# Kernel optimization log

Hardware: AMD Instinct MI355X
Metric: run time of the kernel (lower is better)

Reference implementation:

```python
import jax, jax.numpy as jnp
import numpy as np
import math

B, S, D, H, F, L = 16, 512, 1024, 16, 4096, 4
DK = D // H
NEG = -1e32


def _cosine_pe(max_len, d_model):
    # deterministic sin/cos table (the 0.1*randn init is fully overwritten for even d_model)
    pos = np.arange(max_len, dtype=np.float32)[:, None]
    div = np.exp(np.arange(0, d_model, 2, dtype=np.float32) * (-(math.log(10000.0) / d_model)))
    pe = np.zeros((max_len, d_model), dtype=np.float32)
    pe[:, 0::2] = np.sin(pos * div)
    pe[:, 1::2] = np.cos(pos * div)
    return jnp.asarray(pe)[None]  # [1, max_len, D]


def setup_inputs() -> dict:
    key = jax.random.key(0)
    ks = jax.random.split(key, 16)
    sc_d = 1.0 / math.sqrt(D)
    sc_f = 1.0 / math.sqrt(F)
    return {
        "q_embed_data": jax.random.normal(ks[0], (B, S, D), jnp.float32),
        "qa_embed_data": jax.random.normal(ks[1], (B, S, D), jnp.float32),
        "pe": _cosine_pe(S, D),
        "Wk": jax.random.normal(ks[2], (L, D, D), jnp.float32) * sc_d,
        "bk": jnp.zeros((L, D), jnp.float32),
        "Wv": jax.random.normal(ks[3], (L, D, D), jnp.float32) * sc_d,
        "bv": jnp.zeros((L, D), jnp.float32),
        "Wo": jax.random.normal(ks[4], (L, D, D), jnp.float32) * sc_d,
        "bo": jnp.zeros((L, D), jnp.float32),
        "ln1_g": jnp.ones((L, D), jnp.float32),
        "ln1_b": jnp.zeros((L, D), jnp.float32),
        "W1": jax.random.normal(ks[5], (L, D, F), jnp.float32) * sc_d,
        "b1": jnp.zeros((L, F), jnp.float32),
        "W2": jax.random.normal(ks[6], (L, F, D), jnp.float32) * sc_f,
        "b2": jnp.zeros((L, D), jnp.float32),
        "ln2_g": jnp.ones((L, D), jnp.float32),
        "ln2_b": jnp.zeros((L, D), jnp.float32),
    }


def _layer_norm(x, g, b, eps=1e-5):
    mu = jnp.mean(x, axis=-1, keepdims=True)
    var = jnp.var(x, axis=-1, keepdims=True)
    return (x - mu) * jax.lax.rsqrt(var + eps) * g + b


def _forward(q_embed_data, qa_embed_data, pe, Wk, bk, Wv, bv, Wo, bo,
             ln1_g, ln1_b, W1, b1, W2, b2, ln2_g, ln2_b):
    x = q_embed_data + pe[:, :S, :]
    y = qa_embed_data + pe[:, :S, :]  # values stay fixed across blocks
    # mask=0 in TransformerLayer: triu(k=0)==0 -> strictly-lower-triangular allowed
    allowed = jnp.tril(jnp.ones((S, S), bool), k=-1)  # [S, S]
    row_keep = (jnp.arange(S) > 0).astype(x.dtype)[None, None, :, None]  # zero_pad row 0
    scale = 1.0 / math.sqrt(DK)
    for l in range(L):
        # kq_same: q and k both use k_linear
        qk = (x @ Wk[l] + bk[l]).reshape(B, S, H, DK).transpose(0, 2, 1, 3)  # [B,H,S,DK]
        v = (y @ Wv[l] + bv[l]).reshape(B, S, H, DK).transpose(0, 2, 1, 3)
        scores = jnp.einsum('bhqd,bhkd->bhqk', qk, qk) * scale
        scores = jnp.where(allowed, scores, NEG)
        attn = jax.nn.softmax(scores, axis=-1) * row_keep  # zero_pad: first query row -> zeros
        ctx = jnp.einsum('bhqk,bhkd->bhqd', attn, v)
        ctx = ctx.transpose(0, 2, 1, 3).reshape(B, S, D)
        x = _layer_norm(x + (ctx @ Wo[l] + bo[l]), ln1_g[l], ln1_b[l])
        ffn = jax.nn.relu(x @ W1[l] + b1[l]) @ W2[l] + b2[l]
        x = _layer_norm(x + ffn, ln2_g[l], ln2_b[l])
    return x


def reference(q_embed_data, qa_embed_data, pe, Wk, bk, Wv, bv, Wo, bo,
              ln1_g, ln1_b, W1, b1, W2, b2, ln2_g, ln2_b):
    return _forward(q_embed_data, qa_embed_data, pe, Wk, bk, Wv, bv, Wo, bo,
                    ln1_g, ln1_b, W1, b1, W2, b2, ln2_g, ln2_b)
```

## Files before the change

### kernel.cpp

```cpp
#include <hip/hip_runtime.h>
#include <stdint.h>

typedef unsigned short u16;
typedef __bf16 bf16x8 __attribute__((ext_vector_type(8)));
typedef float f32x4 __attribute__((ext_vector_type(4)));

#define BDIM 16
#define SLEN 512
#define DMODEL 1024
#define NHEAD 16
#define DHEAD 64
#define FDIM 4096
#define NLAYER 4
#define ROWS (BDIM*SLEN)
#define KVT 64

__device__ __forceinline__ u16 f2b(float f) {
  uint32_t u = __builtin_bit_cast(uint32_t, f);
  u = (u + 0x7fffu + ((u >> 16) & 1u)) >> 16;
  return (u16)u;
}
__device__ __forceinline__ float b2f_lo(uint32_t u) {
  return __builtin_bit_cast(float, u << 16);
}
__device__ __forceinline__ float b2f_hi(uint32_t u) {
  return __builtin_bit_cast(float, u & 0xffff0000u);
}

__device__ __forceinline__ void gl_lds16(const void* g, void* l) {
  uint32_t loff = (uint32_t)(uintptr_t)l;
  __builtin_amdgcn_global_load_lds(
      (__attribute__((address_space(1))) uint32_t*)(uintptr_t)g,
      (__attribute__((address_space(3))) uint32_t*)loff,
      16, 0, 0);
}

__global__ __launch_bounds__(256) void prep_kernel(const float4* __restrict__ q,
                                                   const float4* __restrict__ qa,
                                                   const float4* __restrict__ pe,
                                                   float4* __restrict__ x,
                                                   u16* __restrict__ xb,
                                                   u16* __restrict__ yb) {
  int idx = blockIdx.x * 256 + threadIdx.x;
  int pidx = idx & (SLEN * DMODEL / 4 - 1);
  float4 qv = q[idx], av = qa[idx], pv = pe[pidx];
  float4 xv = make_float4(qv.x + pv.x, qv.y + pv.y, qv.z + pv.z, qv.w + pv.w);
  float4 yv = make_float4(av.x + pv.x, av.y + pv.y, av.z + pv.z, av.w + pv.w);
  x[idx] = xv;
  uint32_t x0 = (uint32_t)f2b(xv.x) | ((uint32_t)f2b(xv.y) << 16);
  uint32_t x1 = (uint32_t)f2b(xv.z) | ((uint32_t)f2b(xv.w) << 16);
  uint32_t y0 = (uint32_t)f2b(yv.x) | ((uint32_t)f2b(yv.y) << 16);
  uint32_t y1 = (uint32_t)f2b(yv.z) | ((uint32_t)f2b(yv.w) << 16);
  ((uint2*)xb)[idx] = make_uint2(x0, x1);
  ((uint2*)yb)[idx] = make_uint2(y0, y1);
}

__global__ __launch_bounds__(256) void transpose_f2b(const float* __restrict__ in,
                                                     u16* __restrict__ out,
                                                     int M, int N) {
  __shared__ float t[32][33];
  int tx = threadIdx.x & 31, ty = threadIdx.x >> 5;
  int m0 = blockIdx.y * 32, n0 = blockIdx.x * 32;
  #pragma unroll
  for (int i = 0; i < 32; i += 8) t[ty + i][tx] = in[(size_t)(m0 + ty + i) * N + n0 + tx];
  __syncthreads();
  #pragma unroll
  for (int i = 0; i < 32; i += 8) out[(size_t)(n0 + ty + i) * M + m0 + tx] = f2b(t[tx][ty + i]);
}

template<int BN, bool RELU, bool BF16OUT>
__global__ __launch_bounds__(512, 2) void gemm8p(const u16* __restrict__ Ap,
                                                 const u16* __restrict__ Bp,
                                                 const float* __restrict__ bias,
                                                 void* __restrict__ Cp,
                                                 int M, int N, int K) {
  constexpr int NBH = BN / 128;
  constexpr int NREP = BN / 64;
  constexpr int QN = NREP / 2;
  constexpr int HU = 8192;
  __shared__ __attribute__((aligned(16))) u16 lds[2][(2 + NBH) * HU];

  const int tid = threadIdx.x, wave = tid >> 6, lane = tid & 63;
  const int lg = lane >> 4, lc = lane & 15;
  const int wm = wave >> 2, wn = wave & 3;

  const int gx = gridDim.x;
  int nwg = gx * gridDim.y;
  int orig = blockIdx.y * gx + blockIdx.x;
  int qq = nwg >> 3, rr_ = nwg & 7;
  int xcd = orig & 7, ix = orig >> 3;
  int wg = (xcd < rr_ ? xcd * (qq + 1) : rr_ * (qq + 1) + (xcd - rr_) * qq) + ix;
  const int m0 = (wg / gx) * 256, n0 = (wg % gx) * BN;

  const int ldbyte = K * 2;
  const char* Ag = (const char*)Ap + (size_t)m0 * ldbyte;
  const char* Bg = (const char*)Bp + (size_t)n0 * ldbyte;

  int o1 = tid * 16, o2 = 8192 + tid * 16;
  int sr1 = o1 >> 7, sg1 = (((o1 >> 4) & 7) - sr1) & 7;
  int sr2 = o2 >> 7, sg2 = (((o2 >> 4) & 7) - sr2) & 7;
  const int soff1 = sr1 * ldbyte + sg1 * 16;
  const int soff2 = sr2 * ldbyte + sg2 * 16;
  const int NT = K >> 6;

  auto stageA = [&](int kt, int h, int buf) {
    const char* g = Ag + (size_t)h * 128 * ldbyte + (size_t)kt * 128;
    char* d = (char*)&lds[buf][h * HU] + wave * 1024;
    gl_lds16(g + soff1, d);
    gl_lds16(g + soff2, d + 8192);
  };
  auto stageB = [&](int kt, int h, int buf) {
    const char* g = Bg + (size_t)h * 128 * ldbyte + (size_t)kt * 128;
    char* d = (char*)&lds[buf][(2 + h) * HU] + wave * 1024;
    gl_lds16(g + soff1, d);
    gl_lds16(g + soff2, d + 8192);
  };

  const int bstart = wn * (BN / 4);
  const int bh = bstart >> 7, bc0 = bstart & 127;

  auto rdA = [&](const u16* base, int f, int kk) -> bf16x8 {
    int row = f * 16 + lc;
    return *(const bf16x8*)&base[row * 64 + (((kk * 4 + lg + row) & 7) << 3)];
  };
  auto rdB = [&](const u16* base, int jj, int kk) -> bf16x8 {
    int row = bc0 + jj * 16 + lc;
    return *(const bf16x8*)&base[row * 64 + (((kk * 4 + lg + row) & 7) << 3)];
  };

  f32x4 acc[8][NREP];
  #pragma unroll
  for (int f = 0; f < 8; f++)
    #pragma unroll
    for (int j = 0; j < NREP; j++) acc[f][j] = (f32x4){0.f, 0.f, 0.f, 0.f};

  stageA(0, 0, 0); stageA(0, 1, 0);
  stageB(0, 0, 0); if (NBH == 2) stageB(0, 1, 0);
  stageA(1, 0, 1); stageA(1, 1, 1);
  asm volatile("s_waitcnt vmcnt(4)\n\ts_barrier" ::: "memory");

  auto ktile = [&](int k, int buf) {
    const u16* Ab_ = &lds[buf][wm * HU];
    const u16* Bb_ = &lds[buf][(2 + bh) * HU];
    const int kn = (k + 1 < NT) ? k + 1 : NT - 1;
    const int k2 = (k + 2 < NT) ? k + 2 : NT - 1;
    bf16x8 a0[4][2], a1[4][2], b0[QN][2], b1[QN][2];

    #pragma unroll
    for (int f = 0; f < 4; f++) { a0[f][0] = rdA(Ab_, f, 0); a0[f][1] = rdA(Ab_, f, 1); }
    #pragma unroll
    for (int j = 0; j < QN; j++) { b0[j][0] = rdB(Bb_, j, 0); b0[j][1] = rdB(Bb_, j, 1); }
    stageB(kn, 0, buf ^ 1);
    asm volatile("s_barrier" ::: "memory");
    __builtin_amdgcn_s_setprio(1);
    #pragma unroll
    for (int f = 0; f < 4; f++)
      #pragma unroll
      for (int j = 0; j < QN; j++) {
        acc[f][j] = __builtin_amdgcn_mfma_f32_16x16x32_bf16(a0[f][0], b0[j][0], acc[f][j], 0, 0, 0);
        acc[f][j] = __builtin_amdgcn_mfma_f32_16x16x32_bf16(a0[f][1], b0[j][1], acc[f][j], 0, 0, 0);
      }
    __builtin_amdgcn_s_setprio(0);
    asm volatile("s_barrier" ::: "memory");

    #pragma unroll
    for (int f = 0; f < 4; f++) { a1[f][0] = rdA(Ab_, 4 + f, 0); a1[f][1] = rdA(Ab_, 4 + f, 1); }
    if (NBH == 2) stageB(kn, 1, buf ^ 1);
    asm volatile("s_barrier" ::: "memory");
    __builtin_amdgcn_s_setprio(1);
    #pragma unroll
    for (int f = 0; f < 4; f++)
      #pragma unroll
      for (int j = 0; j < QN; j++) {
        acc[4 + f][j] = __builtin_amdgcn_mfma_f32_16x16x32_bf16(a1[f][0], b0[j][0], acc[4 + f][j], 0, 0, 0);
        acc[4 + f][j] = __builtin_amdgcn_mfma_f32_16x16x32_bf16(a1[f][1], b0[j][1], acc[4 + f][j], 0, 0, 0);
      }
    __builtin_amdgcn_s_setprio(0);
    asm volatile("s_barrier" ::: "memory");

    #pragma unroll
    for (int j = 0; j < QN; j++) { b1[j][0] = rdB(Bb_, QN + j, 0); b1[j][1] = rdB(Bb_, QN + j, 1); }
    stageA(k2, 0, buf);
    asm volatile("s_barrier" ::: "memory");
    __builtin_amdgcn_s_setprio(1);
    #pragma unroll
    for (int f = 0; f < 4; f++)
      #pragma unroll
      for (int j = 0; j < QN; j++) {
        acc[4 + f][QN + j] = __builtin_amdgcn_mfma_f32_16x16x32_bf16(a1[f][0], b1[j][0], acc[4 + f][QN + j], 0, 0, 0);
        acc[4 + f][QN + j] = __builtin_amdgcn_mfma_f32_16x16x32_bf16(a1[f][1], b1[j][1], acc[4 + f][QN + j], 0, 0, 0);
      }
    __builtin_amdgcn_s_setprio(0);
    asm volatile("s_barrier" ::: "memory");

    stageA(k2, 1, buf);
    asm volatile("s_barrier" ::: "memory");
    __builtin_amdgcn_s_setprio(1);
    #pragma unroll
    for (int f = 0; f < 4; f++)
      #pragma unroll
      for (int j = 0; j < QN; j++) {
        acc[f][QN + j] = __builtin_amdgcn_mfma_f32_16x16x32_bf16(a0[f][0], b1[j][0], acc[f][QN + j], 0, 0, 0);
        acc[f][QN + j] = __builtin_amdgcn_mfma_f32_16x16x32_bf16(a0[f][1], b1[j][1], acc[f][QN + j], 0, 0, 0);
      }
    __builtin_amdgcn_s_setprio(0);
    asm volatile("s_waitcnt vmcnt(4)\n\ts_barrier" ::: "memory");
  };

  for (int k = 0; k < NT; k += 2) {
    ktile(k, 0);
    ktile(k + 1, 1);
  }

  #pragma unroll
  for (int f = 0; f < 8; f++) {
    int row = m0 + wm * 128 + f * 16 + lg * 4;
    #pragma unroll
    for (int j = 0; j < NREP; j++) {
      int col = n0 + bstart + j * 16 + lc;
      float bv = bias[col];
      #pragma unroll
      for (int t2 = 0; t2 < 4; t2++) {
        float v = acc[f][j][t2] + bv;
        if (RELU) v = fmaxf(v, 0.f);
        if (BF16OUT) ((u16*)Cp)[(size_t)(row + t2) * N + col] = f2b(v);
        else         ((float*)Cp)[(size_t)(row + t2) * N + col] = v;
      }
    }
  }
}

__global__ __launch_bounds__(256, 2) void gemm4w(const u16* __restrict__ Ap,
                                                 const u16* __restrict__ Bp,
                                                 const float* __restrict__ bias,
                                                 u16* __restrict__ Cp,
                                                 int M, int N, int K) {
  __shared__ __attribute__((aligned(16))) u16 As[2][128 * 64];
  __shared__ __attribute__((aligned(16))) u16 Bs[2][128 * 64];
  const int tid = threadIdx.x, wave = tid >> 6, lane = tid & 63;
  const int lg = lane >> 4, lc = lane & 15;
  const int wm = wave >> 1, wn = wave & 1;

  const int gx = gridDim.x;
  int nwg = gx * gridDim.y;
  int orig = blockIdx.y * gx + blockIdx.x;
  int qq = nwg >> 3, rr_ = nwg & 7;
  int xcd = orig & 7, ix = orig >> 3;
  int wg = (xcd < rr_ ? xcd * (qq + 1) : rr_ * (qq + 1) + (xcd - rr_) * qq) + ix;
  const int m0 = (wg / gx) * 128, n0 = (wg % gx) * 128;

  const int ldbyte = K * 2;
  const char* Ag = (const char*)Ap + (size_t)m0 * ldbyte;
  const char* Bg = (const char*)Bp + (size_t)n0 * ldbyte;
  const int NT = K >> 6;

  auto stage = [&](const char* gb, int kt, u16* lb) {
    #pragma unroll
    for (int c = 0; c < 4; c++) {
      int o = c * 4096 + tid * 16;
      int row = o >> 7;
      int g = (((o >> 4) & 7) - row) & 7;
      gl_lds16(gb + (size_t)row * ldbyte + (size_t)kt * 128 + g * 16,
               (char*)lb + c * 4096 + wave * 1024);
    }
  };
  auto rd = [&](const u16* base, int strip, int f, int kk) -> bf16x8 {
    int row = strip * 64 + f * 16 + lc;
    return *(const bf16x8*)&base[row * 64 + (((kk * 4 + lg + row) & 7) << 3)];
  };

  f32x4 acc[4][4];
  #pragma unroll
  for (int f = 0; f < 4; f++)
    #pragma unroll
    for (int n = 0; n < 4; n++) acc[f][n] = (f32x4){0.f, 0.f, 0.f, 0.f};

  stage(Ag, 0, As[0]); stage(Bg, 0, Bs[0]);
  stage(Ag, 1, As[1]); stage(Bg, 1, Bs[1]);
  asm volatile("s_waitcnt vmcnt(8)\n\ts_barrier" ::: "memory");

  for (int k = 0; k < NT; k++) {
    const int buf = k & 1;
    const int k2 = (k + 2 < NT) ? k + 2 : NT - 1;
    bf16x8 a[4][2], b[4][2];
    #pragma unroll
    for (int f = 0; f < 4; f++) { a[f][0] = rd(As[buf], wm, f, 0); a[f][1] = rd(As[buf], wm, f, 1); }
    #pragma unroll
    for (int n = 0; n < 4; n++) { b[n][0] = rd(Bs[buf], wn, n, 0); b[n][1] = rd(Bs[buf], wn, n, 1); }
    asm volatile("s_barrier" ::: "memory");
    __builtin_amdgcn_s_setprio(1);
    #pragma unroll
    for (int f = 0; f < 4; f++)
      #pragma unroll
      for (int n = 0; n < 2; n++) {
        acc[f][n] = __builtin_amdgcn_mfma_f32_16x16x32_bf16(a[f][0], b[n][0], acc[f][n], 0, 0, 0);
        acc[f][n] = __builtin_amdgcn_mfma_f32_16x16x32_bf16(a[f][1], b[n][1], acc[f][n], 0, 0, 0);
      }
    __builtin_amdgcn_s_setprio(0);
    asm volatile("s_barrier" ::: "memory");
    stage(Ag, k2, As[buf]);
    stage(Bg, k2, Bs[buf]);
    __builtin_amdgcn_s_setprio(1);
    #pragma unroll
    for (int f = 0; f < 4; f++)
      #pragma unroll
      for (int n = 2; n < 4; n++) {
        acc[f][n] = __builtin_amdgcn_mfma_f32_16x16x32_bf16(a[f][0], b[n][0], acc[f][n], 0, 0, 0);
        acc[f][n] = __builtin_amdgcn_mfma_f32_16x16x32_bf16(a[f][1], b[n][1], acc[f][n], 0, 0, 0);
      }
    __builtin_amdgcn_s_setprio(0);
    asm volatile("s_waitcnt vmcnt(8)\n\ts_barrier" ::: "memory");
  }

  #pragma unroll
  for (int f = 0; f < 4; f++) {
    int row = m0 + wm * 64 + f * 16 + lg * 4;
    #pragma unroll
    for (int n = 0; n < 4; n++) {
      int col = n0 + wn * 64 + n * 16 + lc;
      float bv = bias[col];
      #pragma unroll
      for (int r = 0; r < 4; r++)
        Cp[(size_t)(row + r) * N + col] = f2b(acc[f][n][r] + bv);
    }
  }
}

__global__ __launch_bounds__(256, 4) void attn_kernel(const u16* __restrict__ QK,
                                                      const u16* __restrict__ V,
                                                      u16* __restrict__ CTX) {
  __shared__ __attribute__((aligned(16))) u16 Ks[2][KVT * 64];
  __shared__ __attribute__((aligned(16))) u16 VTs[64 * 72];
  __shared__ __attribute__((aligned(16))) u16 Ps[4][16 * 72];
  const int qt = blockIdx.x, bh = blockIdx.y;
  const int b = bh >> 4, h = bh & 15;
  const char* Qg = (const char*)(QK + (size_t)b * SLEN * DMODEL + h * DHEAD);
  const char* Vg = (const char*)(V + (size_t)b * SLEN * DMODEL + h * DHEAD);
  const int tid = threadIdx.x, wave = tid >> 6, lane = tid & 63;
  const int lg = lane >> 4, lc = lane & 15;
  const int ktmax = qt;

  auto stageK = [&](int kt, int buf) {
    #pragma unroll
    for (int i = 0; i < 2; i++) {
      int o = i * 4096 + tid * 16;
      int row = o >> 7, slot = (o >> 4) & 7;
      int g = (slot - row) & 7;
      gl_lds16(Qg + (size_t)(kt * KVT + row) * (DMODEL * 2) + g * 16,
               (char*)Ks[buf] + i * 4096 + wave * 1024);
    }
  };
  const int vhi = lane >> 5, vls = lane & 31;
  const int vc_ = wave + 4 * vhi;
  auto loadV = [&](int kt, uint4 (&va)[2]) {
    const char* src = Vg + (size_t)(kt * KVT + 2 * vls) * (DMODEL * 2) + vc_ * 16;
    va[0] = *(const uint4*)src;
    va[1] = *(const uint4*)(src + DMODEL * 2);
  };
  auto writeVT = [&](const uint4 (&va)[2]) {
    u16 e0[8], e1[8];
    *(uint4*)e0 = va[0];
    *(uint4*)e1 = va[1];
    #pragma unroll
    for (int j = 0; j < 8; j++) {
      uint32_t pk = (uint32_t)e0[j] | ((uint32_t)e1[j] << 16);
      *(uint32_t*)&VTs[(8 * vc_ + j) * 72 + 2 * vls] = pk;
    }
  };

  uint4 vaA[2], vaB[2];
  const int qrow = qt * 64 + wave * 16 + lc;
  bf16x8 aq0 = *(const bf16x8*)(Qg + (size_t)qrow * (DMODEL * 2) + lg * 16);
  bf16x8 aq1 = *(const bf16x8*)(Qg + (size_t)qrow * (DMODEL * 2) + 64 + lg * 16);
  stageK(0, 0);
  loadV(0, vaA);
  stageK(ktmax > 0 ? 1 : 0, 1);
  asm volatile("s_waitcnt vmcnt(2)\n\ts_barrier" ::: "memory");

  float l_run[4] = {0.f, 0.f, 0.f, 0.f};
  f32x4 acc_o[4];
  #pragma unroll
  for (int n = 0; n < 4; n++) acc_o[n] = (f32x4){0.f, 0.f, 0.f, 0.f};

  auto iter = [&](int kt, int cur, uint4 (&vc)[2], uint4 (&vn)[2]) {
    const int kn = (kt + 1 <= ktmax) ? kt + 1 : ktmax;
    const int k2 = (kt + 2 <= ktmax) ? kt + 2 : ktmax;

    asm volatile("s_waitcnt vmcnt(2)" ::: "memory");
    __builtin_amdgcn_s_barrier();
    writeVT(vc);
    loadV(kn, vn);

    f32x4 sc[4];
    #pragma unroll
    for (int n = 0; n < 4; n++) sc[n] = (f32x4){0.f, 0.f, 0.f, 0.f};
    #pragma unroll
    for (int n = 0; n < 4; n++) {
      int row = n * 16 + lc;
      bf16x8 bk0 = *(const bf16x8*)&Ks[cur][row * 64 + (((lg + row) & 7) << 3)];
      bf16x8 bk1 = *(const bf16x8*)&Ks[cur][row * 64 + (((4 + lg + row) & 7) << 3)];
      sc[n] = __builtin_amdgcn_mfma_f32_16x16x32_bf16(aq0, bk0, sc[n], 0, 0, 0);
      sc[n] = __builtin_amdgcn_mfma_f32_16x16x32_bf16(aq1, bk1, sc[n], 0, 0, 0);
    }

    const int qbase = qt * 64 + wave * 16 + lg * 4;
    #pragma unroll
    for (int n = 0; n < 4; n++) {
      int kg = kt * KVT + n * 16 + lc;
      #pragma unroll
      for (int r = 0; r < 4; r++) {
        float e = __expf(fmaf(sc[n][r], 0.125f, -24.f));
        float p = (kg < qbase + r) ? e : 0.f;
        l_run[r] += p;
        Ps[wave][(lg * 4 + r) * 72 + n * 16 + lc] = f2b(p);
      }
    }

    asm volatile("s_waitcnt lgkmcnt(0)" ::: "memory");
    __builtin_amdgcn_s_barrier();
    stageK(k2, cur);

    bf16x8 ap0 = *(const bf16x8*)&Ps[wave][lc * 72 + lg * 8];
    bf16x8 ap1 = *(const bf16x8*)&Ps[wave][lc * 72 + 32 + lg * 8];
    #pragma unroll
    for (int n2 = 0; n2 < 4; n2++) {
      bf16x8 bv0 = *(const bf16x8*)&VTs[(n2 * 16 + lc) * 72 + lg * 8];
      bf16x8 bv1 = *(const bf16x8*)&VTs[(n2 * 16 + lc) * 72 + 32 + lg * 8];
      acc_o[n2] = __builtin_amdgcn_mfma_f32_16x16x32_bf16(ap0, bv0, acc_o[n2], 0, 0, 0);
      acc_o[n2] = __builtin_amdgcn_mfma_f32_16x16x32_bf16(ap1, bv1, acc_o[n2], 0, 0, 0);
    }
  };

  for (int kt = 0; kt <= ktmax; kt += 2) {
    iter(kt, 0, vaA, vaB);
    if (kt + 1 <= ktmax) iter(kt + 1, 1, vaB, vaA);
  }

  #pragma unroll
  for (int d = 1; d < 16; d <<= 1)
    #pragma unroll
    for (int r = 0; r < 4; r++) l_run[r] += __shfl_xor(l_run[r], d, 64);

  asm volatile("s_waitcnt vmcnt(0)" ::: "memory");
  #pragma unroll
  for (int n2 = 0; n2 < 4; n2++)
    #pragma unroll
    for (int r = 0; r < 4; r++) {
      int sq = qt * 64 + wave * 16 + lg * 4 + r;
      float v = (sq == 0) ? 0.f : acc_o[n2][r] / l_run[r];
      CTX[((size_t)b * SLEN + sq) * DMODEL + h * DHEAD + n2 * 16 + lc] = f2b(v);
    }
}

__global__ __launch_bounds__(256) void ln_kernel(const u16* __restrict__ tmp,
                                                 float* __restrict__ x,
                                                 u16* __restrict__ xb,
                                                 const float* __restrict__ gw,
                                                 const float* __restrict__ bw) {
  __shared__ float red[4], red2[4];
  const int row = blockIdx.x, t = threadIdx.x;
  const size_t base = (size_t)row * DMODEL + t * 4;
  float4 xv = *(const float4*)&x[base];
  uint2 tv = *(const uint2*)&tmp[base];
  float v[4];
  v[0] = xv.x + b2f_lo(tv.x); v[1] = xv.y + b2f_hi(tv.x);
  v[2] = xv.z + b2f_lo(tv.y); v[3] = xv.w + b2f_hi(tv.y);
  float s = v[0] + v[1] + v[2] + v[3];
  #pragma unroll
  for (int d = 1; d < 64; d <<= 1) s += __shfl_xor(s, d, 64);
  if ((t & 63) == 0) red[t >> 6] = s;
  __syncthreads();
  float mean = (red[0] + red[1] + red[2] + red[3]) * (1.f / DMODEL);
  float q2 = 0.f;
  #pragma unroll
  for (int i = 0; i < 4; i++) { float d_ = v[i] - mean; q2 += d_ * d_; }
  #pragma unroll
  for (int d = 1; d < 64; d <<= 1) q2 += __shfl_xor(q2, d, 64);
  if ((t & 63) == 0) red2[t >> 6] = q2;
  __syncthreads();
  float var = (red2[0] + red2[1] + red2[2] + red2[3]) * (1.f / DMODEL);
  float rs = rsqrtf(var + 1e-5f);
  float4 gv = *(const float4*)&gw[t * 4];
  float4 bv4 = *(const float4*)&bw[t * 4];
  float o0 = (v[0] - mean) * rs * gv.x + bv4.x;
  float o1 = (v[1] - mean) * rs * gv.y + bv4.y;
  float o2 = (v[2] - mean) * rs * gv.z + bv4.z;
  float o3 = (v[3] - mean) * rs * gv.w + bv4.w;
  *(float4*)&x[base] = make_float4(o0, o1, o2, o3);
  uint2 pk;
  pk.x = (uint32_t)f2b(o0) | ((uint32_t)f2b(o1) << 16);
  pk.y = (uint32_t)f2b(o2) | ((uint32_t)f2b(o3) << 16);
  *(uint2*)&xb[base] = pk;
}

__global__ __launch_bounds__(256) void copy_f4(const float4* __restrict__ src, float4* __restrict__ dst) {
  int i = blockIdx.x * 256 + threadIdx.x;
  dst[i] = src[i];
}

extern "C" void kernel_launch(void* const* d_in, const int* in_sizes, int n_in,
                              void* d_out, int out_size, void* d_ws, size_t ws_size,
                              hipStream_t stream) {
  (void)in_sizes; (void)n_in; (void)out_size; (void)ws_size;
  const float* q    = (const float*)d_in[0];
  const float* qa   = (const float*)d_in[1];
  const float* pe   = (const float*)d_in[2];
  const float* Wk   = (const float*)d_in[3];
  const float* bk   = (const float*)d_in[4];
  const float* Wv   = (const float*)d_in[5];
  const float* bv   = (const float*)d_in[6];
  const float* Wo   = (const float*)d_in[7];
  const float* bo   = (const float*)d_in[8];
  const float* ln1g = (const float*)d_in[9];
  const float* ln1b = (const float*)d_in[10];
  const float* W1   = (const float*)d_in[11];
  const float* b1   = (const float*)d_in[12];
  const float* W2   = (const float*)d_in[13];
  const float* b2   = (const float*)d_in[14];
  const float* ln2g = (const float*)d_in[15];
  const float* ln2b = (const float*)d_in[16];

  char* w = (char*)d_ws;
  float* x_f32 = (float*)w; w += (size_t)ROWS * DMODEL * 4;
  u16* xb   = (u16*)w; w += (size_t)ROWS * DMODEL * 2;
  u16* yb   = (u16*)w; w += (size_t)ROWS * DMODEL * 2;
  u16* qkb  = (u16*)w; w += (size_t)ROWS * DMODEL * 2;
  u16* vb   = (u16*)w; w += (size_t)ROWS * DMODEL * 2;
  u16* ctxb = (u16*)w; w += (size_t)ROWS * DMODEL * 2;
  u16* ffnb = (u16*)w; w += (size_t)ROWS * FDIM * 2;
  u16* WkT  = (u16*)w; w += (size_t)DMODEL * DMODEL * 2;
  u16* WvT  = (u16*)w; w += (size_t)DMODEL * DMODEL * 2;
  u16* WoT  = (u16*)w; w += (size_t)DMODEL * DMODEL * 2;
  u16* W1T  = (u16*)w; w += (size_t)DMODEL * FDIM * 2;
  u16* W2T  = (u16*)w; w += (size_t)DMODEL * FDIM * 2;
  u16* tmpb = qkb;

  prep_kernel<<<ROWS * DMODEL / 4 / 256, 256, 0, stream>>>(
      (const float4*)q, (const float4*)qa, (const float4*)pe, (float4*)x_f32, xb, yb);

  for (int l = 0; l < NLAYER; l++) {
    transpose_f2b<<<dim3(32, 32), 256, 0, stream>>>(Wk + (size_t)l * DMODEL * DMODEL, WkT, DMODEL, DMODEL);
    transpose_f2b<<<dim3(32, 32), 256, 0, stream>>>(Wv + (size_t)l * DMODEL * DMODEL, WvT, DMODEL, DMODEL);
    transpose_f2b<<<dim3(32, 32), 256, 0, stream>>>(Wo + (size_t)l * DMODEL * DMODEL, WoT, DMODEL, DMODEL);
    transpose_f2b<<<dim3(128, 32), 256, 0, stream>>>(W1 + (size_t)l * DMODEL * FDIM, W1T, DMODEL, FDIM);
    transpose_f2b<<<dim3(32, 128), 256, 0, stream>>>(W2 + (size_t)l * FDIM * DMODEL, W2T, FDIM, DMODEL);

    gemm4w<<<dim3(DMODEL / 128, ROWS / 128), 256, 0, stream>>>(
        xb, WkT, bk + l * DMODEL, qkb, ROWS, DMODEL, DMODEL);
    gemm4w<<<dim3(DMODEL / 128, ROWS / 128), 256, 0, stream>>>(
        yb, WvT, bv + l * DMODEL, vb, ROWS, DMODEL, DMODEL);
    attn_kernel<<<dim3(SLEN / 64, BDIM * NHEAD), 256, 0, stream>>>(qkb, vb, ctxb);
    gemm4w<<<dim3(DMODEL / 128, ROWS / 128), 256, 0, stream>>>(
        ctxb, WoT, bo + l * DMODEL, tmpb, ROWS, DMODEL, DMODEL);
    ln_kernel<<<ROWS, 256, 0, stream>>>(tmpb, x_f32, xb, ln1g + l * DMODEL, ln1b + l * DMODEL);
    gemm8p<256, true, true><<<dim3(FDIM / 256, ROWS / 256), 512, 0, stream>>>(
        xb, W1T, b1 + l * FDIM, ffnb, ROWS, FDIM, DMODEL);
    gemm4w<<<dim3(DMODEL / 128, ROWS / 128), 256, 0, stream>>>(
        ffnb, W2T, b2 + l * DMODEL, tmpb, ROWS, DMODEL, FDIM);
    ln_kernel<<<ROWS, 256, 0, stream>>>(tmpb, x_f32, xb, ln2g + l * DMODEL, ln2b + l * DMODEL);
  }
  copy_f4<<<ROWS * DMODEL / 4 / 256, 256, 0, stream>>>((const float4*)x_f32, (float4*)d_out);
}
```

Measured before the change: 1.188 ms.

## Triple-buffer B tiles in 8-wave GEMM and use it for FFN down-projection

The 8-wave ping-pong GEMM now keeps three LDS slots for the weight (B) tile instead of two, so B is prefetched two k-tiles ahead rather than one. Wait counts are adjusted to match the larger number of loads in flight. The FFN second GEMM (K=4096) moves from the 4-wave 128x128 kernel to this 8-wave 256x128 variant. The extra B buffer raises LDS use, which can lower occupancy, and the larger tile halves the workgroup count for the W2 GEMM.

Result: slower. 1.242 ms (+4.5%).

```diff
diff --git a/kernel.cpp b/kernel.cpp
--- a/kernel.cpp
+++ b/kernel.cpp
@@ -68,17 +68,19 @@
   for (int i = 0; i < 32; i += 8) out[(size_t)(n0 + ty + i) * M + m0 + tx] = f2b(t[tx][ty + i]);
 }
 
-template<int BN, bool RELU, bool BF16OUT>
-__global__ __launch_bounds__(512, 2) void gemm8p(const u16* __restrict__ Ap,
-                                                 const u16* __restrict__ Bp,
-                                                 const float* __restrict__ bias,
-                                                 void* __restrict__ Cp,
-                                                 int M, int N, int K) {
+template<int BN, bool RELU>
+__global__ __launch_bounds__(512, 2) void gemm8pd(const u16* __restrict__ Ap,
+                                                  const u16* __restrict__ Bp,
+                                                  const float* __restrict__ bias,
+                                                  u16* __restrict__ Cp,
+                                                  int M, int N, int K) {
   constexpr int NBH = BN / 128;
   constexpr int NREP = BN / 64;
   constexpr int QN = NREP / 2;
   constexpr int HU = 8192;
-  __shared__ __attribute__((aligned(16))) u16 lds[2][(2 + NBH) * HU];
+  constexpr int VW = (2 + NBH) * 2;
+  __shared__ __attribute__((aligned(16))) u16 ldsA[2][2 * HU];
+  __shared__ __attribute__((aligned(16))) u16 ldsB[3][NBH * HU];
 
   const int tid = threadIdx.x, wave = tid >> 6, lane = tid & 63;
   const int lg = lane >> 4, lc = lane & 15;
@@ -105,13 +107,13 @@
 
   auto stageA = [&](int kt, int h, int buf) {
     const char* g = Ag + (size_t)h * 128 * ldbyte + (size_t)kt * 128;
-    char* d = (char*)&lds[buf][h * HU] + wave * 1024;
+    char* d = (char*)&ldsA[buf][h * HU] + wave * 1024;
     gl_lds16(g + soff1, d);
     gl_lds16(g + soff2, d + 8192);
   };
-  auto stageB = [&](int kt, int h, int buf) {
+  auto stageB = [&](int kt, int h, int slot) {
     const char* g = Bg + (size_t)h * 128 * ldbyte + (size_t)kt * 128;
-    char* d = (char*)&lds[buf][(2 + h) * HU] + wave * 1024;
+    char* d = (char*)&ldsB[slot][h * HU] + wave * 1024;
     gl_lds16(g + soff1, d);
     gl_lds16(g + soff2, d + 8192);
   };
@@ -137,12 +139,13 @@
   stageA(0, 0, 0); stageA(0, 1, 0);
   stageB(0, 0, 0); if (NBH == 2) stageB(0, 1, 0);
   stageA(1, 0, 1); stageA(1, 1, 1);
-  asm volatile("s_waitcnt vmcnt(4)\n\ts_barrier" ::: "memory");
-
-  auto ktile = [&](int k, int buf) {
-    const u16* Ab_ = &lds[buf][wm * HU];
-    const u16* Bb_ = &lds[buf][(2 + bh) * HU];
-    const int kn = (k + 1 < NT) ? k + 1 : NT - 1;
+  stageB(1, 0, 1); if (NBH == 2) stageB(1, 1, 1);
+  if (VW == 8) asm volatile("s_waitcnt vmcnt(8)\n\ts_barrier" ::: "memory");
+  else         asm volatile("s_waitcnt vmcnt(6)\n\ts_barrier" ::: "memory");
+
+  auto ktile = [&](int k, int abuf, int bc, int b2) {
+    const u16* Ab_ = &ldsA[abuf][wm * HU];
+    const u16* Bb_ = &ldsB[bc][bh * HU];
     const int k2 = (k + 2 < NT) ? k + 2 : NT - 1;
     bf16x8 a0[4][2], a1[4][2], b0[QN][2], b1[QN][2];
 
@@ -150,7 +153,7 @@
     for (int f = 0; f < 4; f++) { a0[f][0] = rdA(Ab_, f, 0); a0[f][1] = rdA(Ab_, f, 1); }
     #pragma unroll
     for (int j = 0; j < QN; j++) { b0[j][0] = rdB(Bb_, j, 0); b0[j][1] = rdB(Bb_, j, 1); }
-    stageB(kn, 0, buf ^ 1);
+    stageB(k2, 0, b2);
     asm volatile("s_barrier" ::: "memory");
     __builtin_amdgcn_s_setprio(1);
     #pragma unroll
@@ -165,7 +168,7 @@
 
     #pragma unroll
     for (int f = 0; f < 4; f++) { a1[f][0] = rdA(Ab_, 4 + f, 0); a1[f][1] = rdA(Ab_, 4 + f, 1); }
-    if (NBH == 2) stageB(kn, 1, buf ^ 1);
+    if (NBH == 2) stageB(k2, 1, b2);
     asm volatile("s_barrier" ::: "memory");
     __builtin_amdgcn_s_setprio(1);
     #pragma unroll
@@ -180,7 +183,7 @@
 
     #pragma unroll
     for (int j = 0; j < QN; j++) { b1[j][0] = rdB(Bb_, QN + j, 0); b1[j][1] = rdB(Bb_, QN + j, 1); }
-    stageA(k2, 0, buf);
+    stageA(k2, 0, abuf);
     asm volatile("s_barrier" ::: "memory");
     __builtin_amdgcn_s_setprio(1);
     #pragma unroll
@@ -193,7 +196,7 @@
     __builtin_amdgcn_s_setprio(0);
     asm volatile("s_barrier" ::: "memory");
 
-    stageA(k2, 1, buf);
+    stageA(k2, 1, abuf);
     asm volatile("s_barrier" ::: "memory");
     __builtin_amdgcn_s_setprio(1);
     #pragma unroll
@@ -204,12 +207,15 @@
         acc[f][QN + j] = __builtin_amdgcn_mfma_f32_16x16x32_bf16(a0[f][1], b1[j][1], acc[f][QN + j], 0, 0, 0);
       }
     __builtin_amdgcn_s_setprio(0);
-    asm volatile("s_waitcnt vmcnt(4)\n\ts_barrier" ::: "memory");
-  };
-
-  for (int k = 0; k < NT; k += 2) {
-    ktile(k, 0);
-    ktile(k + 1, 1);
+    if (VW == 8) asm volatile("s_waitcnt vmcnt(8)\n\ts_barrier" ::: "memory");
+    else         asm volatile("s_waitcnt vmcnt(6)\n\ts_barrier" ::: "memory");
+  };
+
+  int bc = 0;
+  for (int k = 0; k < NT; k++) {
+    int b2 = bc + 2; if (b2 >= 3) b2 -= 3;
+    ktile(k, k & 1, bc, b2);
+    bc = (bc + 1 == 3) ? 0 : bc + 1;
   }
 
   #pragma unroll
@@ -223,8 +229,7 @@
       for (int t2 = 0; t2 < 4; t2++) {
         float v = acc[f][j][t2] + bv;
         if (RELU) v = fmaxf(v, 0.f);
-        if (BF16OUT) ((u16*)Cp)[(size_t)(row + t2) * N + col] = f2b(v);
-        else         ((float*)Cp)[(size_t)(row + t2) * N + col] = v;
+        Cp[(size_t)(row + t2) * N + col] = f2b(v);
       }
     }
   }
@@ -553,9 +558,9 @@
     gemm4w<<<dim3(DMODEL / 128, ROWS / 128), 256, 0, stream>>>(
         ctxb, WoT, bo + l * DMODEL, tmpb, ROWS, DMODEL, DMODEL);
     ln_kernel<<<ROWS, 256, 0, stream>>>(tmpb, x_f32, xb, ln1g + l * DMODEL, ln1b + l * DMODEL);
-    gemm8p<256, true, true><<<dim3(FDIM / 256, ROWS / 256), 512, 0, stream>>>(
+    gemm8pd<256, true><<<dim3(FDIM / 256, ROWS / 256), 512, 0, stream>>>(
         xb, W1T, b1 + l * FDIM, ffnb, ROWS, FDIM, DMODEL);
-    gemm4w<<<dim3(DMODEL / 128, ROWS / 128), 256, 0, stream>>>(
+    gemm8pd<128, false><<<dim3(DMODEL / 128, ROWS / 256), 512, 0, stream>>>(
         ffnb, W2T, b2 + l * DMODEL, tmpb, ROWS, DMODEL, FDIM);
     ln_kernel<<<ROWS, 256, 0, stream>>>(tmpb, x_f32, xb, ln2g + l * DMODEL, ln2b + l * DMODEL);
   }
```

## Drop fp32 residual stream; fuse residual add into GEMM epilogue using bf16 activations

Applied to the files above, without the earlier changes.

Removes the fp32 copy of the hidden state and keeps only the bf16 version. The residual add moves into the Wo and W2 GEMM epilogues, which read the bf16 activations. LayerNorm then reads a single bf16 tensor and writes only bf16. The final copy becomes a bf16-to-fp32 expansion. This cuts fp32 traffic in prep, LN and the final copy, at the cost of accumulating the residual stream in bf16, which reduces accuracy across layers.

After: 1.173 ms. About the same (-1.3%).

```diff
diff --git a/kernel.cpp b/kernel.cpp
--- a/kernel.cpp
+++ b/kernel.cpp
@@ -20,6 +20,9 @@
   u = (u + 0x7fffu + ((u >> 16) & 1u)) >> 16;
   return (u16)u;
 }
+__device__ __forceinline__ float b2f(u16 u) {
+  return __builtin_bit_cast(float, (uint32_t)u << 16);
+}
 __device__ __forceinline__ float b2f_lo(uint32_t u) {
   return __builtin_bit_cast(float, u << 16);
 }
@@ -38,19 +41,15 @@
 __global__ __launch_bounds__(256) void prep_kernel(const float4* __restrict__ q,
                                                    const float4* __restrict__ qa,
                                                    const float4* __restrict__ pe,
-                                                   float4* __restrict__ x,
                                                    u16* __restrict__ xb,
                                                    u16* __restrict__ yb) {
   int idx = blockIdx.x * 256 + threadIdx.x;
   int pidx = idx & (SLEN * DMODEL / 4 - 1);
   float4 qv = q[idx], av = qa[idx], pv = pe[pidx];
-  float4 xv = make_float4(qv.x + pv.x, qv.y + pv.y, qv.z + pv.z, qv.w + pv.w);
-  float4 yv = make_float4(av.x + pv.x, av.y + pv.y, av.z + pv.z, av.w + pv.w);
-  x[idx] = xv;
-  uint32_t x0 = (uint32_t)f2b(xv.x) | ((uint32_t)f2b(xv.y) << 16);
-  uint32_t x1 = (uint32_t)f2b(xv.z) | ((uint32_t)f2b(xv.w) << 16);
-  uint32_t y0 = (uint32_t)f2b(yv.x) | ((uint32_t)f2b(yv.y) << 16);
-  uint32_t y1 = (uint32_t)f2b(yv.z) | ((uint32_t)f2b(yv.w) << 16);
+  uint32_t x0 = (uint32_t)f2b(qv.x + pv.x) | ((uint32_t)f2b(qv.y + pv.y) << 16);
+  uint32_t x1 = (uint32_t)f2b(qv.z + pv.z) | ((uint32_t)f2b(qv.w + pv.w) << 16);
+  uint32_t y0 = (uint32_t)f2b(av.x + pv.x) | ((uint32_t)f2b(av.y + pv.y) << 16);
+  uint32_t y1 = (uint32_t)f2b(av.z + pv.z) | ((uint32_t)f2b(av.w + pv.w) << 16);
   ((uint2*)xb)[idx] = make_uint2(x0, x1);
   ((uint2*)yb)[idx] = make_uint2(y0, y1);
 }
@@ -230,9 +229,11 @@
   }
 }
 
+template<bool RESID>
 __global__ __launch_bounds__(256, 2) void gemm4w(const u16* __restrict__ Ap,
                                                  const u16* __restrict__ Bp,
                                                  const float* __restrict__ bias,
+                                                 const u16* __restrict__ Rp,
                                                  u16* __restrict__ Cp,
                                                  int M, int N, int K) {
   __shared__ __attribute__((aligned(16))) u16 As[2][128 * 64];
@@ -320,8 +321,11 @@
       int col = n0 + wn * 64 + n * 16 + lc;
       float bv = bias[col];
       #pragma unroll
-      for (int r = 0; r < 4; r++)
-        Cp[(size_t)(row + r) * N + col] = f2b(acc[f][n][r] + bv);
+      for (int r = 0; r < 4; r++) {
+        float v = acc[f][n][r] + bv;
+        if (RESID) v += b2f(Rp[(size_t)(row + r) * N + col]);
+        Cp[(size_t)(row + r) * N + col] = f2b(v);
+      }
     }
   }
 }
@@ -453,18 +457,16 @@
 }
 
 __global__ __launch_bounds__(256) void ln_kernel(const u16* __restrict__ tmp,
-                                                 float* __restrict__ x,
                                                  u16* __restrict__ xb,
                                                  const float* __restrict__ gw,
                                                  const float* __restrict__ bw) {
   __shared__ float red[4], red2[4];
   const int row = blockIdx.x, t = threadIdx.x;
   const size_t base = (size_t)row * DMODEL + t * 4;
-  float4 xv = *(const float4*)&x[base];
   uint2 tv = *(const uint2*)&tmp[base];
   float v[4];
-  v[0] = xv.x + b2f_lo(tv.x); v[1] = xv.y + b2f_hi(tv.x);
-  v[2] = xv.z + b2f_lo(tv.y); v[3] = xv.w + b2f_hi(tv.y);
+  v[0] = b2f_lo(tv.x); v[1] = b2f_hi(tv.x);
+  v[2] = b2f_lo(tv.y); v[3] = b2f_hi(tv.y);
   float s = v[0] + v[1] + v[2] + v[3];
   #pragma unroll
   for (int d = 1; d < 64; d <<= 1) s += __shfl_xor(s, d, 64);
@@ -486,16 +488,17 @@
   float o1 = (v[1] - mean) * rs * gv.y + bv4.y;
   float o2 = (v[2] - mean) * rs * gv.z + bv4.z;
   float o3 = (v[3] - mean) * rs * gv.w + bv4.w;
-  *(float4*)&x[base] = make_float4(o0, o1, o2, o3);
   uint2 pk;
   pk.x = (uint32_t)f2b(o0) | ((uint32_t)f2b(o1) << 16);
   pk.y = (uint32_t)f2b(o2) | ((uint32_t)f2b(o3) << 16);
   *(uint2*)&xb[base] = pk;
 }
 
-__global__ __launch_bounds__(256) void copy_f4(const float4* __restrict__ src, float4* __restrict__ dst) {
+__global__ __launch_bounds__(256) void expand_kernel(const uint2* __restrict__ src,
+                                                     float4* __restrict__ dst) {
   int i = blockIdx.x * 256 + threadIdx.x;
-  dst[i] = src[i];
+  uint2 v = src[i];
+  dst[i] = make_float4(b2f_lo(v.x), b2f_hi(v.x), b2f_lo(v.y), b2f_hi(v.y));
 }
 
 extern "C" void kernel_launch(void* const* d_in, const int* in_sizes, int n_in,
@@ -521,7 +524,6 @@
   const float* ln2b = (const float*)d_in[16];
 
   char* w = (char*)d_ws;
-  float* x_f32 = (float*)w; w += (size_t)ROWS * DMODEL * 4;
   u16* xb   = (u16*)w; w += (size_t)ROWS * DMODEL * 2;
   u16* yb   = (u16*)w; w += (size_t)ROWS * DMODEL * 2;
   u16* qkb  = (u16*)w; w += (size_t)ROWS * DMODEL * 2;
@@ -536,7 +538,7 @@
   u16* tmpb = qkb;
 
   prep_kernel<<<ROWS * DMODEL / 4 / 256, 256, 0, stream>>>(
-      (const float4*)q, (const float4*)qa, (const float4*)pe, (float4*)x_f32, xb, yb);
+      (const float4*)q, (const float4*)qa, (const float4*)pe, xb, yb);
 
   for (int l = 0; l < NLAYER; l++) {
     transpose_f2b<<<dim3(32, 32), 256, 0, stream>>>(Wk + (size_t)l * DMODEL * DMODEL, WkT, DMODEL, DMODEL);
@@ -545,19 +547,19 @@
     transpose_f2b<<<dim3(128, 32), 256, 0, stream>>>(W1 + (size_t)l * DMODEL * FDIM, W1T, DMODEL, FDIM);
     transpose_f2b<<<dim3(32, 128), 256, 0, stream>>>(W2 + (size_t)l * FDIM * DMODEL, W2T, FDIM, DMODEL);
 
-    gemm4w<<<dim3(DMODEL / 128, ROWS / 128), 256, 0, stream>>>(
-        xb, WkT, bk + l * DMODEL, qkb, ROWS, DMODEL, DMODEL);
-    gemm4w<<<dim3(DMODEL / 128, ROWS / 128), 256, 0, stream>>>(
-        yb, WvT, bv + l * DMODEL, vb, ROWS, DMODEL, DMODEL);
+    gemm4w<false><<<dim3(DMODEL / 128, ROWS / 128), 256, 0, stream>>>(
+        xb, WkT, bk + l * DMODEL, nullptr, qkb, ROWS, DMODEL, DMODEL);
+    gemm4w<false><<<dim3(DMODEL / 128, ROWS / 128), 256, 0, stream>>>(
+        yb, WvT, bv + l * DMODEL, nullptr, vb, ROWS, DMODEL, DMODEL);
     attn_kernel<<<dim3(SLEN / 64, BDIM * NHEAD), 256, 0, stream>>>(qkb, vb, ctxb);
-    gemm4w<<<dim3(DMODEL / 128, ROWS / 128), 256, 0, stream>>>(
-        ctxb, WoT, bo + l * DMODEL, tmpb, ROWS, DMODEL, DMODEL);
-    ln_kernel<<<ROWS, 256, 0, stream>>>(tmpb, x_f32, xb, ln1g + l * DMODEL, ln1b + l * DMODEL);
+    gemm4w<true><<<dim3(DMODEL / 128, ROWS / 128), 256, 0, stream>>>(
+        ctxb, WoT, bo + l * DMODEL, xb, tmpb, ROWS, DMODEL, DMODEL);
+    ln_kernel<<<ROWS, 256, 0, stream>>>(tmpb, xb, ln1g + l * DMODEL, ln1b + l * DMODEL);
     gemm8p<256, true, true><<<dim3(FDIM / 256, ROWS / 256), 512, 0, stream>>>(
         xb, W1T, b1 + l * FDIM, ffnb, ROWS, FDIM, DMODEL);
-    gemm4w<<<dim3(DMODEL / 128, ROWS / 128), 256, 0, stream>>>(
-        ffnb, W2T, b2 + l * DMODEL, tmpb, ROWS, DMODEL, FDIM);
-    ln_kernel<<<ROWS, 256, 0, stream>>>(tmpb, x_f32, xb, ln2g + l * DMODEL, ln2b + l * DMODEL);
+    gemm4w<true><<<dim3(DMODEL / 128, ROWS / 128), 256, 0, stream>>>(
+        ffnb, W2T, b2 + l * DMODEL, xb, tmpb, ROWS, DMODEL, FDIM);
+    ln_kernel<<<ROWS, 256, 0, stream>>>(tmpb, xb, ln2g + l * DMODEL, ln2b + l * DMODEL);
   }
-  copy_f4<<<ROWS * DMODEL / 4 / 256, 256, 0, stream>>>((const float4*)x_f32, (float4*)d_out);
-}
+  expand_kernel<<<ROWS * DMODEL / 4 / 256, 256, 0, stream>>>((const uint2*)xb, (float4*)d_out);
+}
```
